# Kernel optimization log

Measured on AMD Instinct MI355X. Metric: run time of the kernel, lower is better.

## Reference

```python
import jax, jax.numpy as jnp
import numpy as np

G, N_REAL, C_IN, C_EDGE, H, D, C_EOUT = 4096, 31, 64, 64, 4, 64, 64
N_NODE = N_REAL + 1  # 32, last local node is the supernode


def setup_inputs() -> dict:
    key = jax.random.key(0)
    # per-graph edge template: bidirectional ring over real nodes (consecutive (u,v),(v,u) pairs),
    # then edges (u, supernode)
    u = np.arange(N_REAL)
    v = (u + 1) % N_REAL
    ring_src = np.stack([u, v], 1).reshape(-1)
    ring_dst = np.stack([v, u], 1).reshape(-1)
    ls = np.concatenate([ring_src, np.arange(N_REAL)])
    ld = np.concatenate([ring_dst, np.full(N_REAL, N_REAL)])
    Eg = ls.shape[0]  # 93
    off = np.arange(G) * N_NODE
    edge_index = np.stack([(off[:, None] + ls[None, :]).reshape(-1),
                           (off[:, None] + ld[None, :]).reshape(-1)])
    N = G * N_NODE
    E = G * Eg
    k1, k2, k3, k4, k5 = jax.random.split(key, 5)
    return {
        "x": jax.random.normal(k1, (N, C_IN), jnp.float32),
        "edge_index": jnp.asarray(edge_index, jnp.int32),
        "edge_inform": jax.random.normal(k2, (E, C_EDGE), jnp.float32) * 0.1,
        "batch": jnp.asarray(np.repeat(np.arange(G), N_NODE), jnp.int32),
        "edge_num": jnp.asarray(np.full(G, Eg), jnp.int32),
        "W_lin_l": jax.random.normal(k3, (C_IN + C_EDGE, H * D), jnp.float32) * 0.05,
        "att_l": jax.random.normal(k4, (1, H, D), jnp.float32) * 0.1,
        "bias": jnp.zeros((D,), jnp.float32),
        "W_ec": jax.random.normal(k5, (C_EDGE, C_EOUT), jnp.float32) * 0.1,
        "b_ec": jnp.zeros((C_EOUT,), jnp.float32),
    }


def reference(x, edge_index, edge_inform, batch, edge_num, W_lin_l, att_l, bias, W_ec, b_ec):
    # graph structure is static metadata -> numpy
    ei = np.asarray(edge_index)
    en = np.asarray(edge_num)
    N = x.shape[0]
    G_ = en.shape[0]
    Eg = int(en[0])
    n = N // G_
    src = jnp.asarray(ei[0])
    dst = jnp.asarray(ei[1])
    Hh, Dd = att_l.shape[1], att_l.shape[2]

    # degree counting (the per-edge python loop in the original)
    deg = jnp.zeros((N,), x.dtype).at[dst].add(1.0)

    # GAT-style edge attention + scatter-sum
    h = jnp.concatenate([x[src], edge_inform], axis=1) @ W_lin_l  # [E, H*D]
    h = h.reshape(-1, Hh, Dd)
    alpha = jax.nn.leaky_relu(jnp.sum(h * att_l, axis=-1))  # [E,H], slope 0.01
    amax = jax.ops.segment_max(alpha, dst, num_segments=N)
    ex = jnp.exp(alpha - amax[dst])
    a = ex / (jax.ops.segment_sum(ex, dst, num_segments=N)[dst] + 1e-16)
    xi = jax.ops.segment_sum(h * a[..., None], dst, num_segments=N)  # [N,H,D]
    out = xi.mean(axis=1) + bias

    # per-graph edge aggregation (structure uniform across graphs by construction)
    le = ei.reshape(2, G_, Eg) - (np.arange(G_) * n)[None, :, None]
    l0, l1 = le[0, 0], le[1, 0]  # local template indices, same for every graph
    midx = np.nonzero((l1 != n - 1) & (l0 != l1))[0]  # mask: drop supernode-dst & self-loops
    even = midx[0::2]
    C = edge_inform.shape[1]
    inf_g = edge_inform.reshape(G_, Eg, C)

    mdst = jnp.asarray(l1[midx])
    eisum = jax.vmap(lambda v: jax.ops.segment_sum(v, mdst, num_segments=n - 1))(inf_g[:, midx])  # [G,n-1,C]

    es, ed = l0[even], l1[even]
    deg_g = deg.reshape(G_, n)
    norm = deg_g[:, es] + deg_g[:, ed] - 2.0  # edge_norm; divide by edge_norm - 1
    temp = (eisum[:, es] + eisum[:, ed] - inf_g[:, even]) / (norm - 1.0)[..., None]  # [G,P,C]
    temps2 = jnp.repeat(temp, 2, axis=1)  # each temp appended twice

    l1_all = jnp.asarray(l1)
    cnt = jnp.zeros((n,), x.dtype).at[l1_all].add(1.0)
    esum_all = jax.vmap(lambda v: jax.ops.segment_sum(v, l1_all, num_segments=n))(inf_g)
    emean = esum_all / cnt[None, :, None]  # scatter reduce='mean'

    gather = jnp.concatenate([temps2, emean, emean[:, : n - 1]], axis=1).reshape(-1, C)
    new_edge_inform = jax.nn.leaky_relu(gather @ W_ec + b_ec)
    return out, new_edge_inform
```

## Files before the change

### kernel.cpp

```cpp
#include <hip/hip_runtime.h>
#include <hip/hip_bf16.h>

#define NUM_G 4096
#define N_REAL 31
#define E_G 93
#define XLS 68
#define OUT2_OFF ((size_t)NUM_G * 32 * 64)

typedef short  short8  __attribute__((ext_vector_type(8)));
typedef float  floatx4 __attribute__((ext_vector_type(4)));

__device__ __forceinline__ float lrelu(float v) { return v > 0.f ? v : 0.01f * v; }

__device__ __forceinline__ int src_of(int e) {
    if (e < 62) { int i = e >> 1; return (e & 1) ? ((i + 1) % 31) : i; }
    return e - 62;
}

__device__ __forceinline__ unsigned short f2bf(float f) {
    __hip_bfloat16 h = __float2bfloat16(f);
    unsigned short u; __builtin_memcpy(&u, &h, 2); return u;
}

__global__ void setup_prep(const float* __restrict__ W, const float* __restrict__ att,
                           const float* __restrict__ Wec,
                           float* __restrict__ vt, __hip_bfloat16* __restrict__ BT,
                           __hip_bfloat16* __restrict__ BT2)
{
    const int t = threadIdx.x, b = blockIdx.x;
    if (b == 0) {
        for (int i = t; i < 512; i += 256) {
            const int k = i >> 2, h = i & 3;
            float acc = 0.f;
            for (int d = 0; d < 64; ++d) acc += W[k * 256 + h * 64 + d] * att[h * 64 + d];
            vt[i] = acc;
        }
    }
    for (int i = b * 4096 + t; i < (b + 1) * 4096; i += 256) {
        const int d = i >> 9, kk = i & 511;
        const int h = kk >> 7, k = kk & 127;
        BT[i] = __float2bfloat16(W[k * 256 + h * 64 + d]);
    }
    for (int i = b * 512 + t; i < b * 512 + 512; i += 256) {
        const int d = i >> 6, k = i & 63;
        BT2[i] = __float2bfloat16(Wec[k * 64 + d]);
    }
}

__global__ __launch_bounds__(256, 2) void fused_main(
    const float* __restrict__ x, const float* __restrict__ einf,
    const float* __restrict__ bias, const float* __restrict__ bec,
    const float* __restrict__ vt, const __hip_bfloat16* __restrict__ BT,
    const __hip_bfloat16* __restrict__ BT2,
    float* __restrict__ out, float* __restrict__ out2)
{
    __shared__ __align__(16) float xl[32 * XLS];
    __shared__ __align__(16) float el[E_G * XLS];
    __shared__ float vl[512];
    __shared__ float al4[96 * 4];
    __shared__ __align__(16) unsigned char U[33280];
    unsigned short* Ap = (unsigned short*)U;
    float*          ul = (float*)U;
    unsigned short* A2 = (unsigned short*)(U + 16384);

    const int t = threadIdx.x;
    const int g = blockIdx.x;
    const int lane = t & 63;
    const int w = t >> 6;
    const int m16 = lane & 15, q = lane >> 4;

    {
        const float4* xg4 = (const float4*)(x + (size_t)g * 2048);
        const float4* eg4 = (const float4*)(einf + (size_t)g * 5952);
        for (int i = t; i < 32 * 16; i += 256)
            ((float4*)(xl + (i >> 4) * XLS))[i & 15] = xg4[i];
        for (int i = t; i < E_G * 16; i += 256)
            ((float4*)(el + (i >> 4) * XLS))[i & 15] = eg4[i];
        vl[t] = vt[t]; vl[t + 256] = vt[t + 256];
    }
    __syncthreads();

    for (int i = t; i < E_G * 4; i += 256) {
        const int e = i >> 2, h = i & 3;
        const int s = src_of(e);
        float acc = 0.f;
        for (int k = 0; k < 64; ++k)
            acc += xl[s * XLS + k] * vl[k * 4 + h] + el[e * XLS + k] * vl[(64 + k) * 4 + h];
        al4[e * 4 + h] = lrelu(acc);
    }
    __syncthreads();

    if (t < 128) {
        const int n = t >> 2, h = t & 3;
        if (n < N_REAL) {
            const int e1 = 2 * ((n + 30) % 31), e2 = 2 * n + 1;
            const float a1 = al4[e1 * 4 + h], a2 = al4[e2 * 4 + h];
            const float m = fmaxf(a1, a2);
            const float x1 = __expf(a1 - m), x2 = __expf(a2 - m);
            const float inv = 1.f / (x1 + x2 + 1e-16f);
            al4[e1 * 4 + h] = x1 * inv;
            al4[e2 * 4 + h] = x2 * inv;
        } else {
            float m = -1e30f;
            for (int i = 0; i < 31; ++i) m = fmaxf(m, al4[(62 + i) * 4 + h]);
            float sden = 1e-16f;
            for (int i = 0; i < 31; ++i) sden += __expf(al4[(62 + i) * 4 + h] - m);
            const float inv = 1.f / sden;
            for (int i = 0; i < 31; ++i)
                al4[(62 + i) * 4 + h] = __expf(al4[(62 + i) * 4 + h] - m) * inv;
        }
    }
    __syncthreads();

    if (t < 248) {
        const int n = t >> 3, h = (t >> 1) & 3, half = t & 1;
        const int e1 = 2 * ((n + 30) % 31), e2 = 2 * n + 1;
        const int s1 = (n + 30) % 31, s2 = (n + 1) % 31;
        const float a1 = al4[e1 * 4 + h], a2 = al4[e2 * 4 + h];
        const float* r1 = half ? (el + e1 * XLS) : (xl + s1 * XLS);
        const float* r2 = half ? (el + e2 * XLS) : (xl + s2 * XLS);
        unsigned short* dst = Ap + n * 520 + h * 128 + half * 64;
        for (int k = 0; k < 64; ++k)
            dst[k] = f2bf(a1 * r1[k] + a2 * r2[k]);
    }
    for (int u = t; u < 512; u += 256) {
        const int h = u >> 7, kp = u & 127;
        const int half = kp >> 6, k = kp & 63;
        float acc = 0.f;
        for (int i = 0; i < 31; ++i) {
            const float a = al4[(62 + i) * 4 + h];
            acc += a * (half ? el[(62 + i) * XLS + k] : xl[i * XLS + k]);
        }
        Ap[31 * 520 + h * 128 + kp] = f2bf(acc);
    }
    __syncthreads();

    {
        floatx4 acc0 = {0.f, 0.f, 0.f, 0.f}, acc1 = {0.f, 0.f, 0.f, 0.f};
        const unsigned short* bt = (const unsigned short*)BT;
        #pragma unroll
        for (int kk = 0; kk < 16; ++kk) {
            short8 b  = *(const short8*)(bt + (w * 16 + m16) * 512 + kk * 32 + q * 8);
            short8 a0 = *(const short8*)(Ap + m16 * 520 + kk * 32 + q * 8);
            short8 a1 = *(const short8*)(Ap + (16 + m16) * 520 + kk * 32 + q * 8);
            acc0 = __builtin_amdgcn_mfma_f32_16x16x32_bf16(a0, b, acc0, 0, 0, 0);
            acc1 = __builtin_amdgcn_mfma_f32_16x16x32_bf16(a1, b, acc1, 0, 0, 0);
        }
        const float bv = bias[w * 16 + m16];
        float* og = out + (size_t)g * 2048;
        #pragma unroll
        for (int r = 0; r < 4; ++r) {
            og[(q * 4 + r) * 64 + w * 16 + m16]      = 0.25f * acc0[r] + bv;
            og[(16 + q * 4 + r) * 64 + w * 16 + m16] = 0.25f * acc1[r] + bv;
        }
    }
    __syncthreads();

    for (int idx = t; idx < 31 * 64; idx += 256) {
        const int j = idx >> 6, cc = idx & 63;
        const int e1 = 2 * ((j + 30) % 31), e2 = 2 * j + 1;
        ul[(31 + j) * 64 + cc] = el[e1 * XLS + cc] + el[e2 * XLS + cc];
    }
    if (t < 64) {
        float s = 0.f;
        for (int i = 0; i < 31; ++i) s += el[(62 + i) * XLS + t];
        ul[62 * 64 + t] = s;
    }
    __syncthreads();

    for (int idx = t; idx < 64 * 64; idx += 256) {
        const int r = idx >> 6, k = idx & 63;
        float v;
        if (r < 31)       v = ul[(31 + r) * 64 + k] + ul[(31 + (r + 1) % 31) * 64 + k]
                              - el[(2 * r) * XLS + k];
        else if (r < 62)  v = 0.5f * ul[r * 64 + k];
        else if (r == 62) v = (1.0f / 31.0f) * ul[62 * 64 + k];
        else              v = 0.f;
        A2[r * 72 + k] = f2bf(v);
    }
    __syncthreads();

    {
        floatx4 z = {0.f, 0.f, 0.f, 0.f};
        floatx4 acc2[4]; acc2[0] = z; acc2[1] = z; acc2[2] = z; acc2[3] = z;
        const unsigned short* bt2 = (const unsigned short*)BT2;
        #pragma unroll
        for (int kk = 0; kk < 2; ++kk) {
            short8 b = *(const short8*)(bt2 + (w * 16 + m16) * 64 + kk * 32 + q * 8);
            #pragma unroll
            for (int mt = 0; mt < 4; ++mt) {
                short8 a = *(const short8*)(A2 + (mt * 16 + m16) * 72 + kk * 32 + q * 8);
                acc2[mt] = __builtin_amdgcn_mfma_f32_16x16x32_bf16(a, b, acc2[mt], 0, 0, 0);
            }
        }
        const int co = w * 16 + m16;
        const float bv2 = bec[co];
        float* o2 = out2 + (size_t)g * 8000;
        #pragma unroll
        for (int mt = 0; mt < 4; ++mt) {
            #pragma unroll
            for (int r = 0; r < 4; ++r) {
                const int row = mt * 16 + q * 4 + r;
                if (row >= 63) continue;
                const float v = lrelu(acc2[mt][r] + bv2);
                if (row < 31) {
                    o2[(2 * row) * 64 + co] = v;
                    o2[(2 * row + 1) * 64 + co] = v;
                } else if (row < 62) {
                    o2[(62 + row - 31) * 64 + co] = v;
                    o2[(94 + row - 31) * 64 + co] = v;
                } else {
                    o2[93 * 64 + co] = v;
                }
            }
        }
    }
}

extern "C" void kernel_launch(void* const* d_in, const int* in_sizes, int n_in,
                              void* d_out, int out_size, void* d_ws, size_t ws_size,
                              hipStream_t stream) {
    const float* x    = (const float*)d_in[0];
    const float* einf = (const float*)d_in[2];
    const float* W    = (const float*)d_in[5];
    const float* att  = (const float*)d_in[6];
    const float* bias = (const float*)d_in[7];
    const float* Wec  = (const float*)d_in[8];
    const float* bec  = (const float*)d_in[9];
    float* out  = (float*)d_out;
    float* out2 = out + OUT2_OFF;

    float* vt            = (float*)d_ws;
    __hip_bfloat16* BT   = (__hip_bfloat16*)((char*)d_ws + 2048);
    __hip_bfloat16* BT2  = (__hip_bfloat16*)((char*)d_ws + 2048 + 65536);

    setup_prep<<<8, 256, 0, stream>>>(W, att, Wec, vt, BT, BT2);
    fused_main<<<NUM_G, 256, 0, stream>>>(x, einf, bias, bec, vt, BT, BT2, out, out2);
}
```

Before: 382.4 us.

## Stage inputs as fp16 in LDS, build attention operands on the fly, raise occupancy

Converts x and edge features to fp16 when staging them into a single compact LDS buffer. This shrinks shared memory enough to allow four blocks per CU. Attention logits are now per-row dot products (packed fp16) that are combined later, and the aggregated A operand is formed in registers inside the MFMA loop rather than materialised in LDS. The kernel also switches from bf16 to fp16 MFMA and computes the edge-feature pass in fp16, which removes a barrier and some LDS traffic but costs range and accuracy in the fp16 accumulations.

```diff
diff --git a/kernel.cpp b/kernel.cpp
--- a/kernel.cpp
+++ b/kernel.cpp
@@ -1,67 +1,56 @@
 #include <hip/hip_runtime.h>
-#include <hip/hip_bf16.h>
+#include <hip/hip_fp16.h>
 
 #define NUM_G 4096
-#define N_REAL 31
-#define E_G 93
-#define XLS 68
+#define RS 72
 #define OUT2_OFF ((size_t)NUM_G * 32 * 64)
 
-typedef short  short8  __attribute__((ext_vector_type(8)));
-typedef float  floatx4 __attribute__((ext_vector_type(4)));
+typedef _Float16 half8  __attribute__((ext_vector_type(8)));
+typedef _Float16 half4v __attribute__((ext_vector_type(4)));
+typedef _Float16 half2v __attribute__((ext_vector_type(2)));
+typedef float    floatx4 __attribute__((ext_vector_type(4)));
 
 __device__ __forceinline__ float lrelu(float v) { return v > 0.f ? v : 0.01f * v; }
-
-__device__ __forceinline__ int src_of(int e) {
-    if (e < 62) { int i = e >> 1; return (e & 1) ? ((i + 1) % 31) : i; }
-    return e - 62;
-}
-
-__device__ __forceinline__ unsigned short f2bf(float f) {
-    __hip_bfloat16 h = __float2bfloat16(f);
-    unsigned short u; __builtin_memcpy(&u, &h, 2); return u;
-}
 
 __global__ void setup_prep(const float* __restrict__ W, const float* __restrict__ att,
                            const float* __restrict__ Wec,
-                           float* __restrict__ vt, __hip_bfloat16* __restrict__ BT,
-                           __hip_bfloat16* __restrict__ BT2)
+                           _Float16* __restrict__ vp, _Float16* __restrict__ BT,
+                           _Float16* __restrict__ BT2)
 {
     const int t = threadIdx.x, b = blockIdx.x;
     if (b == 0) {
         for (int i = t; i < 512; i += 256) {
-            const int k = i >> 2, h = i & 3;
+            const int h8 = i >> 6, k = i & 63;
+            const int h = h8 & 3, ro = (h8 < 4) ? 0 : 64;
             float acc = 0.f;
-            for (int d = 0; d < 64; ++d) acc += W[k * 256 + h * 64 + d] * att[h * 64 + d];
-            vt[i] = acc;
+            for (int d = 0; d < 64; ++d) acc += W[(ro + k) * 256 + h * 64 + d] * att[h * 64 + d];
+            vp[i] = (_Float16)acc;
         }
     }
     for (int i = b * 4096 + t; i < (b + 1) * 4096; i += 256) {
-        const int d = i >> 9, kk = i & 511;
-        const int h = kk >> 7, k = kk & 127;
-        BT[i] = __float2bfloat16(W[k * 256 + h * 64 + d]);
+        const int d = i >> 9, kk = i & 511, h = kk >> 7, k = kk & 127;
+        BT[i] = (_Float16)W[k * 256 + h * 64 + d];
     }
     for (int i = b * 512 + t; i < b * 512 + 512; i += 256) {
         const int d = i >> 6, k = i & 63;
-        BT2[i] = __float2bfloat16(Wec[k * 64 + d]);
+        BT2[i] = (_Float16)Wec[k * 64 + d];
     }
 }
 
-__global__ __launch_bounds__(256, 2) void fused_main(
+__global__ __launch_bounds__(256, 4) void fused_main(
     const float* __restrict__ x, const float* __restrict__ einf,
     const float* __restrict__ bias, const float* __restrict__ bec,
-    const float* __restrict__ vt, const __hip_bfloat16* __restrict__ BT,
-    const __hip_bfloat16* __restrict__ BT2,
+    const _Float16* __restrict__ vp, const _Float16* __restrict__ BT,
+    const _Float16* __restrict__ BT2,
     float* __restrict__ out, float* __restrict__ out2)
 {
-    __shared__ __align__(16) float xl[32 * XLS];
-    __shared__ __align__(16) float el[E_G * XLS];
-    __shared__ float vl[512];
-    __shared__ float al4[96 * 4];
-    __shared__ __align__(16) unsigned char U[33280];
-    unsigned short* Ap = (unsigned short*)U;
-    float*          ul = (float*)U;
-    unsigned short* A2 = (unsigned short*)(U + 16384);
+    __shared__ __align__(16) _Float16 R[128 * RS];
+    __shared__ __align__(16) unsigned char U[9216];
+    _Float16* vpl  = (_Float16*)U;
+    float*    sal  = (float*)(U + 1152);
+    _Float16* virt = (_Float16*)(U + 5760);
+    float*    al4  = (float*)(U + 6784);
+    _Float16* A2   = (_Float16*)U;
 
     const int t = threadIdx.x;
     const int g = blockIdx.x;
@@ -71,30 +60,46 @@
 
     {
         const float4* xg4 = (const float4*)(x + (size_t)g * 2048);
+        for (int i = t; i < 512; i += 256) {
+            float4 v = xg4[i];
+            half4v h4 = {(_Float16)v.x, (_Float16)v.y, (_Float16)v.z, (_Float16)v.w};
+            *(half4v*)(R + (i >> 4) * RS + (i & 15) * 4) = h4;
+        }
         const float4* eg4 = (const float4*)(einf + (size_t)g * 5952);
-        for (int i = t; i < 32 * 16; i += 256)
-            ((float4*)(xl + (i >> 4) * XLS))[i & 15] = xg4[i];
-        for (int i = t; i < E_G * 16; i += 256)
-            ((float4*)(el + (i >> 4) * XLS))[i & 15] = eg4[i];
-        vl[t] = vt[t]; vl[t + 256] = vt[t + 256];
-    }
-    __syncthreads();
-
-    for (int i = t; i < E_G * 4; i += 256) {
-        const int e = i >> 2, h = i & 3;
-        const int s = src_of(e);
-        float acc = 0.f;
-        for (int k = 0; k < 64; ++k)
-            acc += xl[s * XLS + k] * vl[k * 4 + h] + el[e * XLS + k] * vl[(64 + k) * 4 + h];
-        al4[e * 4 + h] = lrelu(acc);
+        for (int i = t; i < 1488; i += 256) {
+            float4 v = eg4[i];
+            half4v h4 = {(_Float16)v.x, (_Float16)v.y, (_Float16)v.z, (_Float16)v.w};
+            *(half4v*)(R + (32 + (i >> 4)) * RS + (i & 15) * 4) = h4;
+        }
+        for (int i = t; i < 512; i += 256)
+            vpl[(i >> 6) * RS + (i & 63)] = vp[i];
+    }
+    __syncthreads();
+
+    #pragma unroll
+    for (int j = 0; j < 4; ++j) {
+        const int combo = t + 256 * j;
+        const int r = combo >> 3, h8 = combo & 7;
+        const _Float16* rr = R + r * RS;
+        const _Float16* vr = vpl + h8 * RS;
+        half8 a8 = {0, 0, 0, 0, 0, 0, 0, 0};
+        #pragma unroll
+        for (int k8 = 0; k8 < 8; ++k8)
+            a8 += (*(const half8*)(rr + k8 * 8)) * (*(const half8*)(vr + k8 * 8));
+        float s = 0.f;
+        #pragma unroll
+        for (int jj = 0; jj < 8; ++jj) s += (float)a8[jj];
+        sal[r * 9 + h8] = s;
     }
     __syncthreads();
 
     if (t < 128) {
         const int n = t >> 2, h = t & 3;
-        if (n < N_REAL) {
-            const int e1 = 2 * ((n + 30) % 31), e2 = 2 * n + 1;
-            const float a1 = al4[e1 * 4 + h], a2 = al4[e2 * 4 + h];
+        if (n < 31) {
+            const int s1 = (n + 30) % 31, s2 = (n + 1) % 31;
+            const int e1 = 2 * s1, e2 = 2 * n + 1;
+            const float a1 = lrelu(sal[s1 * 9 + h] + sal[(32 + e1) * 9 + 4 + h]);
+            const float a2 = lrelu(sal[s2 * 9 + h] + sal[(32 + e2) * 9 + 4 + h]);
             const float m = fmaxf(a1, a2);
             const float x1 = __expf(a1 - m), x2 = __expf(a2 - m);
             const float inv = 1.f / (x1 + x2 + 1e-16f);
@@ -102,95 +107,115 @@
             al4[e2 * 4 + h] = x2 * inv;
         } else {
             float m = -1e30f;
-            for (int i = 0; i < 31; ++i) m = fmaxf(m, al4[(62 + i) * 4 + h]);
+            for (int i = 0; i < 31; ++i)
+                m = fmaxf(m, lrelu(sal[i * 9 + h] + sal[(94 + i) * 9 + 4 + h]));
             float sden = 1e-16f;
-            for (int i = 0; i < 31; ++i) sden += __expf(al4[(62 + i) * 4 + h] - m);
+            for (int i = 0; i < 31; ++i)
+                sden += __expf(lrelu(sal[i * 9 + h] + sal[(94 + i) * 9 + 4 + h]) - m);
             const float inv = 1.f / sden;
             for (int i = 0; i < 31; ++i)
-                al4[(62 + i) * 4 + h] = __expf(al4[(62 + i) * 4 + h] - m) * inv;
-        }
-    }
-    __syncthreads();
-
-    if (t < 248) {
-        const int n = t >> 3, h = (t >> 1) & 3, half = t & 1;
-        const int e1 = 2 * ((n + 30) % 31), e2 = 2 * n + 1;
-        const int s1 = (n + 30) % 31, s2 = (n + 1) % 31;
-        const float a1 = al4[e1 * 4 + h], a2 = al4[e2 * 4 + h];
-        const float* r1 = half ? (el + e1 * XLS) : (xl + s1 * XLS);
-        const float* r2 = half ? (el + e2 * XLS) : (xl + s2 * XLS);
-        unsigned short* dst = Ap + n * 520 + h * 128 + half * 64;
-        for (int k = 0; k < 64; ++k)
-            dst[k] = f2bf(a1 * r1[k] + a2 * r2[k]);
-    }
-    for (int u = t; u < 512; u += 256) {
-        const int h = u >> 7, kp = u & 127;
-        const int half = kp >> 6, k = kp & 63;
+                al4[(62 + i) * 4 + h] =
+                    __expf(lrelu(sal[i * 9 + h] + sal[(94 + i) * 9 + 4 + h]) - m) * inv;
+        }
+    }
+    __syncthreads();
+
+    #pragma unroll
+    for (int j = 0; j < 2; ++j) {
+        const int c = t + 256 * j;
+        const int h = c >> 7, hf = (c >> 6) & 1, k = c & 63;
         float acc = 0.f;
-        for (int i = 0; i < 31; ++i) {
-            const float a = al4[(62 + i) * 4 + h];
-            acc += a * (half ? el[(62 + i) * XLS + k] : xl[i * XLS + k]);
-        }
-        Ap[31 * 520 + h * 128 + kp] = f2bf(acc);
-    }
-    __syncthreads();
-
-    {
+        for (int i = 0; i < 31; ++i)
+            acc += al4[(62 + i) * 4 + h] * (float)R[(hf ? 94 + i : i) * RS + k];
+        virt[c] = (_Float16)acc;
+    }
+    __syncthreads();
+
+    {
+        const int n0 = m16, n1 = 16 + m16;
+        const int n1c = (n1 < 31) ? n1 : 30;
+        const int s1_0 = (n0 + 30) % 31, s2_0 = (n0 + 1) % 31;
+        const int e1_0 = 2 * s1_0, e2_0 = 2 * n0 + 1;
+        const int s1_1 = (n1c + 30) % 31, s2_1 = (n1c + 1) % 31;
+        const int e1_1 = 2 * s1_1, e2_1 = 2 * n1c + 1;
+        _Float16 a1_0[4], a2_0[4], a1_1[4], a2_1[4];
+        #pragma unroll
+        for (int h = 0; h < 4; ++h) {
+            a1_0[h] = (_Float16)al4[e1_0 * 4 + h];
+            a2_0[h] = (_Float16)al4[e2_0 * 4 + h];
+            a1_1[h] = (_Float16)al4[e1_1 * 4 + h];
+            a2_1[h] = (_Float16)al4[e2_1 * 4 + h];
+        }
+        const int co = w * 16 + m16;
         floatx4 acc0 = {0.f, 0.f, 0.f, 0.f}, acc1 = {0.f, 0.f, 0.f, 0.f};
-        const unsigned short* bt = (const unsigned short*)BT;
         #pragma unroll
         for (int kk = 0; kk < 16; ++kk) {
-            short8 b  = *(const short8*)(bt + (w * 16 + m16) * 512 + kk * 32 + q * 8);
-            short8 a0 = *(const short8*)(Ap + m16 * 520 + kk * 32 + q * 8);
-            short8 a1 = *(const short8*)(Ap + (16 + m16) * 520 + kk * 32 + q * 8);
-            acc0 = __builtin_amdgcn_mfma_f32_16x16x32_bf16(a0, b, acc0, 0, 0, 0);
-            acc1 = __builtin_amdgcn_mfma_f32_16x16x32_bf16(a1, b, acc1, 0, 0, 0);
-        }
-        const float bv = bias[w * 16 + m16];
+            const int h = kk >> 2, hf = (kk >> 1) & 1;
+            const int k0 = (kk & 1) * 32 + q * 8;
+            const int r1_0 = hf ? 32 + e1_0 : s1_0, r2_0 = hf ? 32 + e2_0 : s2_0;
+            const int r1_1 = hf ? 32 + e1_1 : s1_1, r2_1 = hf ? 32 + e2_1 : s2_1;
+            half8 b = *(const half8*)(BT + co * 512 + kk * 32 + q * 8);
+            half8 x1 = *(const half8*)(R + r1_0 * RS + k0);
+            half8 x2 = *(const half8*)(R + r2_0 * RS + k0);
+            half8 af0 = x1 * a1_0[h] + x2 * a2_0[h];
+            acc0 = __builtin_amdgcn_mfma_f32_16x16x32_f16(af0, b, acc0, 0, 0, 0);
+            half8 y1 = *(const half8*)(R + r1_1 * RS + k0);
+            half8 y2 = *(const half8*)(R + r2_1 * RS + k0);
+            half8 af1 = y1 * a1_1[h] + y2 * a2_1[h];
+            half8 vv = *(const half8*)(virt + kk * 32 + q * 8);
+            af1 = (m16 == 15) ? vv : af1;
+            acc1 = __builtin_amdgcn_mfma_f32_16x16x32_f16(af1, b, acc1, 0, 0, 0);
+        }
+        const float bv = bias[co];
         float* og = out + (size_t)g * 2048;
         #pragma unroll
         for (int r = 0; r < 4; ++r) {
-            og[(q * 4 + r) * 64 + w * 16 + m16]      = 0.25f * acc0[r] + bv;
-            og[(16 + q * 4 + r) * 64 + w * 16 + m16] = 0.25f * acc1[r] + bv;
-        }
-    }
-    __syncthreads();
-
-    for (int idx = t; idx < 31 * 64; idx += 256) {
-        const int j = idx >> 6, cc = idx & 63;
-        const int e1 = 2 * ((j + 30) % 31), e2 = 2 * j + 1;
-        ul[(31 + j) * 64 + cc] = el[e1 * XLS + cc] + el[e2 * XLS + cc];
-    }
-    if (t < 64) {
-        float s = 0.f;
-        for (int i = 0; i < 31; ++i) s += el[(62 + i) * XLS + t];
-        ul[62 * 64 + t] = s;
-    }
-    __syncthreads();
-
-    for (int idx = t; idx < 64 * 64; idx += 256) {
-        const int r = idx >> 6, k = idx & 63;
-        float v;
-        if (r < 31)       v = ul[(31 + r) * 64 + k] + ul[(31 + (r + 1) % 31) * 64 + k]
-                              - el[(2 * r) * XLS + k];
-        else if (r < 62)  v = 0.5f * ul[r * 64 + k];
-        else if (r == 62) v = (1.0f / 31.0f) * ul[62 * 64 + k];
-        else              v = 0.f;
-        A2[r * 72 + k] = f2bf(v);
+            og[(q * 4 + r) * 64 + co]        = 0.25f * acc0[r] + bv;
+            og[(16 + q * 4 + r) * 64 + co]   = 0.25f * acc1[r] + bv;
+        }
+    }
+
+    half8 b2a = *(const half8*)(BT2 + (w * 16 + m16) * 64 + 0 * 32 + q * 8);
+    half8 b2b = *(const half8*)(BT2 + (w * 16 + m16) * 64 + 1 * 32 + q * 8);
+    __syncthreads();
+
+    {
+        const _Float16* E = R + 32 * RS;
+        for (int idx = t; idx < 62 * 32; idx += 256) {
+            const int r = idx >> 5, k = (idx & 31) * 2;
+            half2v v;
+            if (r < 31) {
+                const int ra = 2 * ((r + 30) % 31), rb = 2 * r + 1, rc = 2 * ((r + 1) % 31) + 1;
+                v = *(const half2v*)(E + ra * RS + k) + *(const half2v*)(E + rb * RS + k)
+                  + *(const half2v*)(E + rc * RS + k);
+            } else {
+                const int jj = r - 31;
+                const int ra = 2 * ((jj + 30) % 31), rb = 2 * jj + 1;
+                v = (*(const half2v*)(E + ra * RS + k) + *(const half2v*)(E + rb * RS + k))
+                    * (_Float16)0.5f;
+            }
+            *(half2v*)(A2 + r * RS + k) = v;
+        }
+        if (t < 64) {
+            float s = 0.f;
+            for (int i = 0; i < 31; ++i) s += (float)E[(62 + i) * RS + t];
+            A2[62 * RS + t] = (_Float16)(s * (1.f / 31.f));
+        } else if (t < 128) {
+            A2[63 * RS + (t - 64)] = (_Float16)0.f;
+        }
     }
     __syncthreads();
 
     {
         floatx4 z = {0.f, 0.f, 0.f, 0.f};
         floatx4 acc2[4]; acc2[0] = z; acc2[1] = z; acc2[2] = z; acc2[3] = z;
-        const unsigned short* bt2 = (const unsigned short*)BT2;
         #pragma unroll
         for (int kk = 0; kk < 2; ++kk) {
-            short8 b = *(const short8*)(bt2 + (w * 16 + m16) * 64 + kk * 32 + q * 8);
+            half8 b = kk ? b2b : b2a;
             #pragma unroll
             for (int mt = 0; mt < 4; ++mt) {
-                short8 a = *(const short8*)(A2 + (mt * 16 + m16) * 72 + kk * 32 + q * 8);
-                acc2[mt] = __builtin_amdgcn_mfma_f32_16x16x32_bf16(a, b, acc2[mt], 0, 0, 0);
+                half8 a = *(const half8*)(A2 + (mt * 16 + m16) * RS + kk * 32 + q * 8);
+                acc2[mt] = __builtin_amdgcn_mfma_f32_16x16x32_f16(a, b, acc2[mt], 0, 0, 0);
             }
         }
         const int co = w * 16 + m16;
@@ -204,7 +229,7 @@
                 if (row >= 63) continue;
                 const float v = lrelu(acc2[mt][r] + bv2);
                 if (row < 31) {
-                    o2[(2 * row) * 64 + co] = v;
+                    o2[(2 * row) * 64 + co]     = v;
                     o2[(2 * row + 1) * 64 + co] = v;
                 } else if (row < 62) {
                     o2[(62 + row - 31) * 64 + co] = v;
@@ -230,10 +255,10 @@
     float* out  = (float*)d_out;
     float* out2 = out + OUT2_OFF;
 
-    float* vt            = (float*)d_ws;
-    __hip_bfloat16* BT   = (__hip_bfloat16*)((char*)d_ws + 2048);
-    __hip_bfloat16* BT2  = (__hip_bfloat16*)((char*)d_ws + 2048 + 65536);
-
-    setup_prep<<<8, 256, 0, stream>>>(W, att, Wec, vt, BT, BT2);
-    fused_main<<<NUM_G, 256, 0, stream>>>(x, einf, bias, bec, vt, BT, BT2, out, out2);
+    _Float16* vp  = (_Float16*)d_ws;
+    _Float16* BT  = (_Float16*)((char*)d_ws + 1024);
+    _Float16* BT2 = (_Float16*)((char*)d_ws + 1024 + 65536);
+
+    setup_prep<<<8, 256, 0, stream>>>(W, att, Wec, vp, BT, BT2);
+    fused_main<<<NUM_G, 256, 0, stream>>>(x, einf, bias, bec, vp, BT, BT2, out, out2);
 }
```

Result: faster. 326.0 us (-14.7%).
